# Optimization experiments

Measured on AMD Instinct MI355X. Metric: run time of the kernel, lower is better.

## Reference

```python
import jax, jax.numpy as jnp
import numpy as np

IN_DIM = 128
OUT_DIM = 128
N_NODES = 10000
N_EDGES = 640000


def setup_inputs() -> dict:
    key = jax.random.key(0)
    ks = jax.random.split(key, 9)
    X = jax.random.normal(ks[0], (N_NODES, IN_DIM), dtype=jnp.float32)
    edge_index = jax.random.randint(ks[1], (2, N_EDGES), 0, N_NODES, dtype=jnp.int64)
    edge_types = jax.random.randint(ks[2], (N_EDGES,), 0, 2, dtype=jnp.int64)
    s = 1.0 / np.sqrt(IN_DIM)
    W_data = jax.random.uniform(ks[3], (OUT_DIM, IN_DIM), minval=-s, maxval=s, dtype=jnp.float32)
    b_data = jax.random.uniform(ks[4], (OUT_DIM,), minval=-s, maxval=s, dtype=jnp.float32)
    W_control = jax.random.uniform(ks[5], (OUT_DIM, IN_DIM), minval=-s, maxval=s, dtype=jnp.float32)
    b_control = jax.random.uniform(ks[6], (OUT_DIM,), minval=-s, maxval=s, dtype=jnp.float32)
    W_self = jax.random.uniform(ks[7], (OUT_DIM, IN_DIM), minval=-s, maxval=s, dtype=jnp.float32)
    b_self = jax.random.uniform(ks[8], (OUT_DIM,), minval=-s, maxval=s, dtype=jnp.float32)
    return {"X": X, "edge_index": edge_index, "edge_types": edge_types,
            "W_data": W_data, "b_data": b_data,
            "W_control": W_control, "b_control": b_control,
            "W_self": W_self, "b_self": b_self}


def reference(X, edge_index, edge_types, W_data, b_data, W_control, b_control, W_self, b_self):
    src, dst = edge_index[0], edge_index[1]
    Xs = X[src]                               # [E, in_dim] gather
    m_data = Xs @ W_data.T + b_data           # [E, out_dim]
    m_ctrl = Xs @ W_control.T + b_control     # [E, out_dim]
    msg = jnp.where((edge_types == 0)[:, None], m_data, m_ctrl)
    agg = jax.ops.segment_sum(msg, dst, num_segments=X.shape[0])  # scatter-add to dst
    out = agg + (X @ W_self.T + b_self)
    return jax.nn.relu(out)
```

## Files before the change

### kernel.cpp

```cpp
#include <hip/hip_runtime.h>


#define IN_DIM 128
#define K_CAT  384
#define CAP    256
#define CSTR   16

typedef short short8  __attribute__((ext_vector_type(8)));
typedef float floatx4 __attribute__((ext_vector_type(4)));

__device__ inline unsigned short f2bf(float f) {
    unsigned u = __float_as_uint(f);
    u += 0x7FFF + ((u >> 16) & 1);
    return (unsigned short)(u >> 16);
}

__global__ __launch_bounds__(256) void append_kernel(
    const int* __restrict__ src,
    const int* __restrict__ dst,
    const int* __restrict__ etype,
    int* __restrict__ cnt,
    unsigned short* __restrict__ bucket, int E)
{
    int e = blockIdx.x * 256 + threadIdx.x;
    if (e >= E) return;
    int d = dst[e];
    int pos = atomicAdd(&cnt[d * CSTR], 1);
    if (pos < CAP) {
        bucket[(size_t)d * CAP + pos] =
            (unsigned short)(src[e] | (etype[e] << 15));
    }
}

__global__ __launch_bounds__(256) void accum_kernel(
    const float* __restrict__ X,
    const int* __restrict__ cnt,
    const unsigned short* __restrict__ bucket,
    unsigned short* __restrict__ AC,
    float* __restrict__ c0, float* __restrict__ c1,
    int N)
{
    const int sub = threadIdx.x >> 5;
    const int q   = threadIdx.x & 31;
    const int d   = blockIdx.x * 8 + sub;
    if (d >= N) return;

    const float4* X4 = (const float4*)X;

    int len = cnt[d * CSTR];
    if (len > CAP) len = CAP;

    float4 a0 = make_float4(0.f, 0.f, 0.f, 0.f);
    float4 a1 = make_float4(0.f, 0.f, 0.f, 0.f);
    int n0 = 0;

    const unsigned short* bl = bucket + (size_t)d * CAP;

#define PROC(P) do {                                                     \
        int _p = (int)(P);                                               \
        int _s = _p & 0x7FFF;                                            \
        int _t = _p >> 15;                                               \
        float4 _v = X4[_s * 32 + q];                                     \
        float _m0 = _t ? 0.f : 1.f;                                      \
        float _m1 = 1.f - _m0;                                           \
        a0.x = fmaf(_v.x, _m0, a0.x); a1.x = fmaf(_v.x, _m1, a1.x);      \
        a0.y = fmaf(_v.y, _m0, a0.y); a1.y = fmaf(_v.y, _m1, a1.y);      \
        a0.z = fmaf(_v.z, _m0, a0.z); a1.z = fmaf(_v.z, _m1, a1.z);      \
        a0.w = fmaf(_v.w, _m0, a0.w); a1.w = fmaf(_v.w, _m1, a1.w);      \
        n0 += 1 - _t;                                                    \
    } while (0)

    int i = 0;
    for (; i + 8 <= len; i += 8) {
        uint4 pp = *(const uint4*)(bl + i);
        PROC(pp.x & 0xFFFF); PROC(pp.x >> 16);
        PROC(pp.y & 0xFFFF); PROC(pp.y >> 16);
        PROC(pp.z & 0xFFFF); PROC(pp.z >> 16);
        PROC(pp.w & 0xFFFF); PROC(pp.w >> 16);
    }
    for (; i < len; i++) PROC(bl[i]);
#undef PROC

    float4 vx = X4[d * 32 + q];

    unsigned short* row = AC + (size_t)d * K_CAT;
    ushort4 o;
    o.x = f2bf(a0.x); o.y = f2bf(a0.y); o.z = f2bf(a0.z); o.w = f2bf(a0.w);
    *(ushort4*)(row + q * 4) = o;
    o.x = f2bf(a1.x); o.y = f2bf(a1.y); o.z = f2bf(a1.z); o.w = f2bf(a1.w);
    *(ushort4*)(row + 128 + q * 4) = o;
    o.x = f2bf(vx.x); o.y = f2bf(vx.y); o.z = f2bf(vx.z); o.w = f2bf(vx.w);
    *(ushort4*)(row + 256 + q * 4) = o;

    if (q == 0) {
        c0[d] = (float)n0;
        c1[d] = (float)(len - n0);
    }
}

__global__ __launch_bounds__(256) void wcat_kernel(
    const float* __restrict__ Wd, const float* __restrict__ Wc,
    const float* __restrict__ Ws,
    unsigned short* __restrict__ Wcat)
{
    int idx = blockIdx.x * 256 + threadIdx.x;
    if (idx >= 128 * K_CAT) return;
    int o = idx / K_CAT;
    int k = idx - o * K_CAT;
    float v = (k < 128) ? Wd[o * 128 + k]
            : (k < 256) ? Wc[o * 128 + (k - 128)]
                        : Ws[o * 128 + (k - 256)];
    Wcat[idx] = f2bf(v);
}

__global__ __launch_bounds__(256) void mfma_gemm_kernel(
    const unsigned short* __restrict__ AC,
    const unsigned short* __restrict__ Wcat,
    const float* __restrict__ c0, const float* __restrict__ c1,
    const float* __restrict__ bd, const float* __restrict__ bc,
    const float* __restrict__ bs,
    float* __restrict__ out, int N)
{
    const int wave = threadIdx.x >> 6;
    const int lane = threadIdx.x & 63;
    const int tile = blockIdx.x * 4 + wave;
    const int m0   = tile * 16;
    if (m0 >= N) return;

    const int rA   = lane & 15;
    const int quad = lane >> 4;

    int arow = m0 + rA;
    if (arow >= N) arow = N - 1;

    const short8* A8 = (const short8*)(AC + (size_t)arow * K_CAT);
    const short8* W8 = (const short8*)Wcat;

    floatx4 acc[8];
    #pragma unroll
    for (int nt = 0; nt < 8; nt++) acc[nt] = (floatx4){0.f, 0.f, 0.f, 0.f};

    #pragma unroll 2
    for (int kt = 0; kt < 12; kt++) {
        short8 a = A8[kt * 4 + quad];
        #pragma unroll
        for (int nt = 0; nt < 8; nt++) {
            short8 b = W8[(nt * 16 + rA) * 48 + kt * 4 + quad];
            acc[nt] = __builtin_amdgcn_mfma_f32_16x16x32_bf16(a, b, acc[nt], 0, 0, 0);
        }
    }

    float c0v[4], c1v[4];
    #pragma unroll
    for (int r = 0; r < 4; r++) {
        int row = m0 + quad * 4 + r;
        if (row >= N) row = N - 1;
        c0v[r] = c0[row]; c1v[r] = c1[row];
    }
    #pragma unroll
    for (int nt = 0; nt < 8; nt++) {
        int col = nt * 16 + rA;
        float bdv = bd[col], bcv = bc[col], bsv = bs[col];
        #pragma unroll
        for (int r = 0; r < 4; r++) {
            int row = m0 + quad * 4 + r;
            if (row < N) {
                float v = acc[nt][r] + c0v[r] * bdv + c1v[r] * bcv + bsv;
                out[(size_t)row * 128 + col] = fmaxf(v, 0.f);
            }
        }
    }
}

extern "C" void kernel_launch(void* const* d_in, const int* in_sizes, int n_in,
                              void* d_out, int out_size, void* d_ws, size_t ws_size,
                              hipStream_t stream) {
    const float* X  = (const float*)d_in[0];
    const int*   ei = (const int*)d_in[1];
    const int*   et = (const int*)d_in[2];
    const float* Wd = (const float*)d_in[3];
    const float* bd = (const float*)d_in[4];
    const float* Wc = (const float*)d_in[5];
    const float* bc = (const float*)d_in[6];
    const float* Ws = (const float*)d_in[7];
    const float* bs = (const float*)d_in[8];
    float* out = (float*)d_out;

    const int N = in_sizes[0] / IN_DIM;
    const int E = in_sizes[2];

    unsigned short* AC     = (unsigned short*)d_ws;
    unsigned short* Wcat   = AC + (size_t)N * K_CAT;
    unsigned short* bucket = Wcat + 128 * K_CAT;
    float* c0   = (float*)(bucket + (size_t)N * CAP);
    float* c1   = c0 + N;
    int*   cnt  = (int*)(c1 + N);

    const int* src = ei;
    const int* dst = ei + E;

    hipMemsetAsync(cnt, 0, (size_t)N * CSTR * sizeof(int), stream);

    wcat_kernel<<<(128 * K_CAT + 255) / 256, 256, 0, stream>>>(Wd, Wc, Ws, Wcat);

    int eb = (E + 255) / 256;
    append_kernel<<<eb, 256, 0, stream>>>(src, dst, et, cnt, bucket, E);

    int ab = (N + 7) / 8;
    accum_kernel<<<ab, 256, 0, stream>>>(X, cnt, bucket, AC, c0, c1, N);

    int tiles = (N + 15) / 16;
    int gb = (tiles + 3) / 4;
    mfma_gemm_kernel<<<gb, 256, 0, stream>>>(
        AC, Wcat, c0, c1, bd, bc, bs, out, N);
}
```

Baseline: 158.3 us.

## Fuse neighbor accumulation with MFMA GEMM via shared-memory A tile

Merges the accumulation kernel and the MFMA GEMM into one kernel: each 512-thread block aggregates 16 destination rows into a padded LDS tile, then 8 waves each compute one 16-column output tile from it. The weight matrix is pre-packed into MFMA fragment order so each lane loads its B operand with one contiguous vector read. This removes the global round trip of the bf16 concatenated activations and the per-node counts, and drops one kernel launch. The cost is a block-wide barrier between the gather phase and the GEMM phase, and the gather loop is unrolled to 16 edges per iteration.

After: 136.9 us. 13.5% less time.

```diff
diff --git a/kernel.cpp b/kernel.cpp
--- a/kernel.cpp
+++ b/kernel.cpp
@@ -5,6 +5,7 @@
 #define K_CAT  384
 #define CAP    256
 #define CSTR   16
+#define ROWP   392
 
 typedef short short8  __attribute__((ext_vector_type(8)));
 typedef float floatx4 __attribute__((ext_vector_type(4)));
@@ -32,142 +33,134 @@
     }
 }
 
-__global__ __launch_bounds__(256) void accum_kernel(
+__global__ __launch_bounds__(256) void wcatT_kernel(
+    const float* __restrict__ Wd, const float* __restrict__ Wc,
+    const float* __restrict__ Ws,
+    unsigned short* __restrict__ WB)
+{
+    int idx = blockIdx.x * 256 + threadIdx.x;
+    if (idx >= 8 * 12 * 64) return;
+    int lane = idx & 63;
+    int kt   = (idx >> 6) % 12;
+    int nt   = idx / (64 * 12);
+    int col  = nt * 16 + (lane & 15);
+    int kb   = kt * 32 + (lane >> 4) * 8;
+    unsigned short v[8];
+    #pragma unroll
+    for (int j = 0; j < 8; j++) {
+        int k = kb + j;
+        float w = (k < 128) ? Wd[col * 128 + k]
+                : (k < 256) ? Wc[col * 128 + (k - 128)]
+                            : Ws[col * 128 + (k - 256)];
+        v[j] = f2bf(w);
+    }
+    *(short8*)(WB + (size_t)idx * 8) = *(short8*)v;
+}
+
+__global__ __launch_bounds__(512) void fused_kernel(
     const float* __restrict__ X,
     const int* __restrict__ cnt,
     const unsigned short* __restrict__ bucket,
-    unsigned short* __restrict__ AC,
-    float* __restrict__ c0, float* __restrict__ c1,
-    int N)
-{
-    const int sub = threadIdx.x >> 5;
-    const int q   = threadIdx.x & 31;
-    const int d   = blockIdx.x * 8 + sub;
-    if (d >= N) return;
-
-    const float4* X4 = (const float4*)X;
-
-    int len = cnt[d * CSTR];
-    if (len > CAP) len = CAP;
-
-    float4 a0 = make_float4(0.f, 0.f, 0.f, 0.f);
-    float4 a1 = make_float4(0.f, 0.f, 0.f, 0.f);
-    int n0 = 0;
-
-    const unsigned short* bl = bucket + (size_t)d * CAP;
-
-#define PROC(P) do {                                                     \
-        int _p = (int)(P);                                               \
-        int _s = _p & 0x7FFF;                                            \
-        int _t = _p >> 15;                                               \
-        float4 _v = X4[_s * 32 + q];                                     \
-        float _m0 = _t ? 0.f : 1.f;                                      \
-        float _m1 = 1.f - _m0;                                           \
-        a0.x = fmaf(_v.x, _m0, a0.x); a1.x = fmaf(_v.x, _m1, a1.x);      \
-        a0.y = fmaf(_v.y, _m0, a0.y); a1.y = fmaf(_v.y, _m1, a1.y);      \
-        a0.z = fmaf(_v.z, _m0, a0.z); a1.z = fmaf(_v.z, _m1, a1.z);      \
-        a0.w = fmaf(_v.w, _m0, a0.w); a1.w = fmaf(_v.w, _m1, a1.w);      \
-        n0 += 1 - _t;                                                    \
-    } while (0)
-
-    int i = 0;
-    for (; i + 8 <= len; i += 8) {
-        uint4 pp = *(const uint4*)(bl + i);
-        PROC(pp.x & 0xFFFF); PROC(pp.x >> 16);
-        PROC(pp.y & 0xFFFF); PROC(pp.y >> 16);
-        PROC(pp.z & 0xFFFF); PROC(pp.z >> 16);
-        PROC(pp.w & 0xFFFF); PROC(pp.w >> 16);
-    }
-    for (; i < len; i++) PROC(bl[i]);
-#undef PROC
-
-    float4 vx = X4[d * 32 + q];
-
-    unsigned short* row = AC + (size_t)d * K_CAT;
-    ushort4 o;
-    o.x = f2bf(a0.x); o.y = f2bf(a0.y); o.z = f2bf(a0.z); o.w = f2bf(a0.w);
-    *(ushort4*)(row + q * 4) = o;
-    o.x = f2bf(a1.x); o.y = f2bf(a1.y); o.z = f2bf(a1.z); o.w = f2bf(a1.w);
-    *(ushort4*)(row + 128 + q * 4) = o;
-    o.x = f2bf(vx.x); o.y = f2bf(vx.y); o.z = f2bf(vx.z); o.w = f2bf(vx.w);
-    *(ushort4*)(row + 256 + q * 4) = o;
-
-    if (q == 0) {
-        c0[d] = (float)n0;
-        c1[d] = (float)(len - n0);
-    }
-}
-
-__global__ __launch_bounds__(256) void wcat_kernel(
-    const float* __restrict__ Wd, const float* __restrict__ Wc,
-    const float* __restrict__ Ws,
-    unsigned short* __restrict__ Wcat)
-{
-    int idx = blockIdx.x * 256 + threadIdx.x;
-    if (idx >= 128 * K_CAT) return;
-    int o = idx / K_CAT;
-    int k = idx - o * K_CAT;
-    float v = (k < 128) ? Wd[o * 128 + k]
-            : (k < 256) ? Wc[o * 128 + (k - 128)]
-                        : Ws[o * 128 + (k - 256)];
-    Wcat[idx] = f2bf(v);
-}
-
-__global__ __launch_bounds__(256) void mfma_gemm_kernel(
-    const unsigned short* __restrict__ AC,
-    const unsigned short* __restrict__ Wcat,
-    const float* __restrict__ c0, const float* __restrict__ c1,
+    const unsigned short* __restrict__ WB,
     const float* __restrict__ bd, const float* __restrict__ bc,
     const float* __restrict__ bs,
     float* __restrict__ out, int N)
 {
-    const int wave = threadIdx.x >> 6;
-    const int lane = threadIdx.x & 63;
-    const int tile = blockIdx.x * 4 + wave;
-    const int m0   = tile * 16;
-    if (m0 >= N) return;
-
+    __shared__ unsigned short Als[16][ROWP];
+    __shared__ float lc0[16], lc1[16];
+
+    const int tid = threadIdx.x;
+    const int m0  = blockIdx.x * 16;
+
+    {
+        const int hw = tid >> 5;
+        const int q  = tid & 31;
+        const int d  = m0 + hw;
+        if (d < N) {
+            const float4* X4 = (const float4*)X;
+            int len = cnt[d * CSTR];
+            if (len > CAP) len = CAP;
+
+            float4 a0 = make_float4(0.f, 0.f, 0.f, 0.f);
+            float4 a1 = make_float4(0.f, 0.f, 0.f, 0.f);
+            int n0 = 0;
+            const unsigned short* bl = bucket + (size_t)d * CAP;
+
+#define PROC(P) do {                                                     \
+            int _p = (int)(P);                                           \
+            int _s = _p & 0x7FFF;                                        \
+            int _t = _p >> 15;                                           \
+            float4 _v = X4[_s * 32 + q];                                 \
+            float _m0 = _t ? 0.f : 1.f;                                  \
+            float _m1 = 1.f - _m0;                                       \
+            a0.x = fmaf(_v.x, _m0, a0.x); a1.x = fmaf(_v.x, _m1, a1.x);  \
+            a0.y = fmaf(_v.y, _m0, a0.y); a1.y = fmaf(_v.y, _m1, a1.y);  \
+            a0.z = fmaf(_v.z, _m0, a0.z); a1.z = fmaf(_v.z, _m1, a1.z);  \
+            a0.w = fmaf(_v.w, _m0, a0.w); a1.w = fmaf(_v.w, _m1, a1.w);  \
+            n0 += 1 - _t;                                                \
+        } while (0)
+#define PROC8(PP) do {                                                   \
+            PROC((PP).x & 0xFFFF); PROC((PP).x >> 16);                   \
+            PROC((PP).y & 0xFFFF); PROC((PP).y >> 16);                   \
+            PROC((PP).z & 0xFFFF); PROC((PP).z >> 16);                   \
+            PROC((PP).w & 0xFFFF); PROC((PP).w >> 16);                   \
+        } while (0)
+
+            int i = 0;
+            for (; i + 16 <= len; i += 16) {
+                uint4 p0 = *(const uint4*)(bl + i);
+                uint4 p1 = *(const uint4*)(bl + i + 8);
+                PROC8(p0); PROC8(p1);
+            }
+            for (; i + 8 <= len; i += 8) {
+                uint4 p0 = *(const uint4*)(bl + i);
+                PROC8(p0);
+            }
+            for (; i < len; i++) PROC(bl[i]);
+#undef PROC8
+#undef PROC
+
+            float4 vx = X4[d * 32 + q];
+            unsigned short* row = &Als[hw][0];
+            ushort4 o;
+            o.x = f2bf(a0.x); o.y = f2bf(a0.y); o.z = f2bf(a0.z); o.w = f2bf(a0.w);
+            *(ushort4*)(row + q * 4) = o;
+            o.x = f2bf(a1.x); o.y = f2bf(a1.y); o.z = f2bf(a1.z); o.w = f2bf(a1.w);
+            *(ushort4*)(row + 128 + q * 4) = o;
+            o.x = f2bf(vx.x); o.y = f2bf(vx.y); o.z = f2bf(vx.z); o.w = f2bf(vx.w);
+            *(ushort4*)(row + 256 + q * 4) = o;
+            if (q == 0) {
+                lc0[hw] = (float)n0;
+                lc1[hw] = (float)(len - n0);
+            }
+        }
+    }
+    __syncthreads();
+
+    const int wave = tid >> 6;
+    const int lane = tid & 63;
     const int rA   = lane & 15;
     const int quad = lane >> 4;
 
-    int arow = m0 + rA;
-    if (arow >= N) arow = N - 1;
-
-    const short8* A8 = (const short8*)(AC + (size_t)arow * K_CAT);
-    const short8* W8 = (const short8*)Wcat;
-
-    floatx4 acc[8];
+    floatx4 acc = (floatx4){0.f, 0.f, 0.f, 0.f};
+    const short8* B8 = (const short8*)WB + (size_t)wave * 12 * 64 + lane;
+
     #pragma unroll
-    for (int nt = 0; nt < 8; nt++) acc[nt] = (floatx4){0.f, 0.f, 0.f, 0.f};
-
-    #pragma unroll 2
     for (int kt = 0; kt < 12; kt++) {
-        short8 a = A8[kt * 4 + quad];
-        #pragma unroll
-        for (int nt = 0; nt < 8; nt++) {
-            short8 b = W8[(nt * 16 + rA) * 48 + kt * 4 + quad];
-            acc[nt] = __builtin_amdgcn_mfma_f32_16x16x32_bf16(a, b, acc[nt], 0, 0, 0);
-        }
-    }
-
-    float c0v[4], c1v[4];
+        short8 a = *(const short8*)&Als[rA][kt * 32 + quad * 8];
+        short8 b = B8[kt * 64];
+        acc = __builtin_amdgcn_mfma_f32_16x16x32_bf16(a, b, acc, 0, 0, 0);
+    }
+
+    const int col = wave * 16 + rA;
+    const float bdv = bd[col], bcv = bc[col], bsv = bs[col];
     #pragma unroll
     for (int r = 0; r < 4; r++) {
-        int row = m0 + quad * 4 + r;
-        if (row >= N) row = N - 1;
-        c0v[r] = c0[row]; c1v[r] = c1[row];
-    }
-    #pragma unroll
-    for (int nt = 0; nt < 8; nt++) {
-        int col = nt * 16 + rA;
-        float bdv = bd[col], bcv = bc[col], bsv = bs[col];
-        #pragma unroll
-        for (int r = 0; r < 4; r++) {
-            int row = m0 + quad * 4 + r;
-            if (row < N) {
-                float v = acc[nt][r] + c0v[r] * bdv + c1v[r] * bcv + bsv;
-                out[(size_t)row * 128 + col] = fmaxf(v, 0.f);
-            }
+        int lrow = quad * 4 + r;
+        int grow = m0 + lrow;
+        if (grow < N) {
+            float v = acc[r] + lc0[lrow] * bdv + lc1[lrow] * bcv + bsv;
+            out[(size_t)grow * 128 + col] = fmaxf(v, 0.f);
         }
     }
 }
@@ -189,28 +182,20 @@
     const int N = in_sizes[0] / IN_DIM;
     const int E = in_sizes[2];
 
-    unsigned short* AC     = (unsigned short*)d_ws;
-    unsigned short* Wcat   = AC + (size_t)N * K_CAT;
-    unsigned short* bucket = Wcat + 128 * K_CAT;
-    float* c0   = (float*)(bucket + (size_t)N * CAP);
-    float* c1   = c0 + N;
-    int*   cnt  = (int*)(c1 + N);
+    unsigned short* WB     = (unsigned short*)d_ws;
+    unsigned short* bucket = WB + (size_t)8 * 12 * 64 * 8;
+    int*            cnt    = (int*)(bucket + (size_t)N * CAP);
 
     const int* src = ei;
     const int* dst = ei + E;
 
     hipMemsetAsync(cnt, 0, (size_t)N * CSTR * sizeof(int), stream);
 
-    wcat_kernel<<<(128 * K_CAT + 255) / 256, 256, 0, stream>>>(Wd, Wc, Ws, Wcat);
+    wcatT_kernel<<<(8 * 12 * 64 + 255) / 256, 256, 0, stream>>>(Wd, Wc, Ws, WB);
 
     int eb = (E + 255) / 256;
     append_kernel<<<eb, 256, 0, stream>>>(src, dst, et, cnt, bucket, E);
 
-    int ab = (N + 7) / 8;
-    accum_kernel<<<ab, 256, 0, stream>>>(X, cnt, bucket, AC, c0, c1, N);
-
-    int tiles = (N + 15) / 16;
-    int gb = (tiles + 3) / 4;
-    mfma_gemm_kernel<<<gb, 256, 0, stream>>>(
-        AC, Wcat, c0, c1, bd, bc, bs, out, N);
-}
+    int fb = (N + 15) / 16;
+    fused_kernel<<<fb, 512, 0, stream>>>(X, cnt, bucket, WB, bd, bc, bs, out, N);
+}
```
